# Optimization experiments

Measured on AMD Instinct MI355X. Metric: run time of the kernel, lower is better.

The kernel has to match this reference:

```python
import jax, jax.numpy as jnp
import numpy as np

# Fixed-step Dormand-Prince RK45 (dopri5) over t in [0, 1].
# torchdiffeq's dopri5 is adaptive; an adaptive while-loop is not
# reverse-differentiable in JAX, so we use the same dopri5 tableau with a
# fixed step count, which reproduces the per-step math exactly.
N_STEPS = 64

# dopri5 Butcher tableau (a-matrix rows; b = 5th-order weights = row a7)
A21 = 1/5
A31, A32 = 3/40, 9/40
A41, A42, A43 = 44/45, -56/15, 32/9
A51, A52, A53, A54 = 19372/6561, -25360/2187, 64448/6561, -212/729
A61, A62, A63, A64, A65 = 9017/3168, -355/33, 46732/5247, 49/176, -5103/18656
B1, B3, B4, B5, B6 = 35/384, 500/1113, 125/192, -2187/6784, 11/84


def setup_inputs() -> dict:
    key = jax.random.key(0)
    ks = jax.random.split(key, 7)
    data_dim, hidden_dim, batch = 512, 1024, 4096
    s1 = 1.0 / np.sqrt(data_dim)
    s2 = 1.0 / np.sqrt(hidden_dim)
    return {
        "x":  jax.random.normal(ks[0], (batch, data_dim), jnp.float32),
        "W1": jax.random.normal(ks[1], (hidden_dim, data_dim), jnp.float32) * s1,
        "b1": jax.random.normal(ks[2], (hidden_dim,), jnp.float32) * s1,
        "W2": jax.random.normal(ks[3], (hidden_dim, hidden_dim), jnp.float32) * s2,
        "b2": jax.random.normal(ks[4], (hidden_dim,), jnp.float32) * s2,
        "W3": jax.random.normal(ks[5], (data_dim, hidden_dim), jnp.float32) * s2,
        "b3": jax.random.normal(ks[6], (data_dim,), jnp.float32) * s2,
    }


def reference(x, W1, b1, W2, b2, W3, b3):
    def f(y):  # ODEFunc MLP: fc1 -> relu -> fc2 -> relu -> fc3 (autonomous)
        h = jax.nn.relu(y @ W1.T + b1)
        h = jax.nn.relu(h @ W2.T + b2)
        return h @ W3.T + b3

    h = jnp.float32(1.0 / N_STEPS)

    def step(y, _):
        k1 = f(y)
        k2 = f(y + h * (A21 * k1))
        k3 = f(y + h * (A31 * k1 + A32 * k2))
        k4 = f(y + h * (A41 * k1 + A42 * k2 + A43 * k3))
        k5 = f(y + h * (A51 * k1 + A52 * k2 + A53 * k3 + A54 * k4))
        k6 = f(y + h * (A61 * k1 + A62 * k2 + A63 * k3 + A64 * k4 + A65 * k5))
        y_next = y + h * (B1 * k1 + B3 * k3 + B4 * k4 + B5 * k5 + B6 * k6)
        return y_next, None

    y_final, _ = jax.lax.scan(step, x, None, length=N_STEPS)
    return y_final
```

## Files before the change

kernel.cpp:

```cpp
#include <hip/hip_runtime.h>
#include <hip/hip_bf16.h>
#include <stdint.h>
#include <stddef.h>

using bf16_t = __hip_bfloat16;
typedef __attribute__((ext_vector_type(8))) short short8;
typedef __attribute__((ext_vector_type(4))) float f32x4;

__device__ __forceinline__ void gload_lds16(void* lds, const void* g) {
  __builtin_amdgcn_global_load_lds(
      (const __attribute__((address_space(1))) unsigned int*)g,
      (__attribute__((address_space(3))) unsigned int*)lds,
      16, 0, 0);
}

template<int MODE>
__device__ __forceinline__ void gemm_core(
    const bf16_t* __restrict__ A, const bf16_t* __restrict__ B,
    const float* __restrict__ bias,
    bf16_t* __restrict__ obf,
    bf16_t* __restrict__ aux,
    bf16_t* __restrict__ vout,
    float* __restrict__ wacc,
    float* __restrict__ yf_out,
    const float* __restrict__ y_in,
    const bf16_t* __restrict__ p0, const bf16_t* __restrict__ p1,
    const bf16_t* __restrict__ p2, const bf16_t* __restrict__ p3,
    float c0, float c1, float c2, float c3, float ccur, int hinit,
    int M, int N, int K, int lgx)
{
  __shared__ __align__(16) bf16_t As[2][64 * 64];
  __shared__ __align__(16) bf16_t Bs[2][64 * 64];

  const int t    = threadIdx.x;
  const int lane = t & 63;
  const int wid  = t >> 6;
  const int wm   = wid >> 1;
  const int wn   = wid & 1;

  const int nwg = gridDim.x, bid = blockIdx.x;
  const int swz = (bid & 7) * (nwg >> 3) + (bid >> 3);
  const int gxm = (1 << lgx) - 1;
  const int bx  = swz & gxm;
  const int by  = swz >> lgx;
  const int bn0 = bx * 64, bm0 = by * 64;

  const bf16_t* Ag = A + (size_t)bm0 * K;
  const bf16_t* Bg = B + (size_t)bn0 * K;

  f32x4 acc[2][2] = {};

  auto stage = [&](int b, int kt) {
    const int k0 = kt * 64;
#pragma unroll
    for (int r = 0; r < 2; ++r) {
      int ch  = t + r * 256;
      int row = ch >> 3, s = ch & 7;
      int sl  = s ^ (row & 7);
      gload_lds16(&As[b][ch * 8], Ag + (size_t)row * K + k0 + sl * 8);
    }
#pragma unroll
    for (int r = 0; r < 2; ++r) {
      int ch  = t + r * 256;
      int row = ch >> 3, s = ch & 7;
      int sl  = s ^ (row & 7);
      gload_lds16(&Bs[b][ch * 8], Bg + (size_t)row * K + k0 + sl * 8);
    }
  };

  const int nt = K >> 6;
  stage(0, 0);

  const int ro = lane & 15;
  const int ks = lane >> 4;

  for (int tt = 0; tt < nt; ++tt) {
    const int c = tt & 1;
    asm volatile("s_waitcnt vmcnt(0)" ::: "memory");
    __builtin_amdgcn_s_barrier();
    asm volatile("" ::: "memory");
    if (tt + 1 < nt) stage(c ^ 1, tt + 1);

#pragma unroll
    for (int kk = 0; kk < 2; ++kk) {
      short8 af[2], bfr[2];
      const int slot = kk * 4 + ks;
#pragma unroll
      for (int mi = 0; mi < 2; ++mi) {
        int row = wm * 32 + mi * 16 + ro;
        int ch  = row * 8 + (slot ^ (row & 7));
        af[mi]  = *(const short8*)&As[c][ch * 8];
      }
#pragma unroll
      for (int ni = 0; ni < 2; ++ni) {
        int row = wn * 32 + ni * 16 + ro;
        int ch  = row * 8 + (slot ^ (row & 7));
        bfr[ni] = *(const short8*)&Bs[c][ch * 8];
      }
      __builtin_amdgcn_s_setprio(1);
#pragma unroll
      for (int mi = 0; mi < 2; ++mi)
#pragma unroll
        for (int ni = 0; ni < 2; ++ni)
          acc[mi][ni] = __builtin_amdgcn_mfma_f32_16x16x32_bf16(
              af[mi], bfr[ni], acc[mi][ni], 0, 0, 0);
      __builtin_amdgcn_s_setprio(0);
    }
  }

  const int rb = bm0 + wm * 32;
  const int cb = bn0 + wn * 32;
#pragma unroll
  for (int mi = 0; mi < 2; ++mi) {
#pragma unroll
    for (int ni = 0; ni < 2; ++ni) {
      const int col = cb + ni * 16 + ro;
      const float bv = bias ? bias[col] : 0.f;
#pragma unroll
      for (int r = 0; r < 4; ++r) {
        const int row = rb + mi * 16 + (lane >> 4) * 4 + r;
        const size_t idx = (size_t)row * N + col;
        const float a = acc[mi][ni][r];
        if (MODE == 0) {
          float v = fmaxf(a + bv, 0.f);
          obf[idx] = __float2bfloat16(v);
          if (aux) {
            float hs = ccur * v + (hinit ? 0.f : __bfloat162float(aux[idx]));
            aux[idx] = __float2bfloat16(hs);
          }
        } else if (MODE == 1) {
          vout[idx] = __float2bfloat16(a);
          float u = wacc[idx] + ccur * a + bv;
          if (p0) u += c0 * __bfloat162float(p0[idx]);
          if (p1) u += c1 * __bfloat162float(p1[idx]);
          if (p2) u += c2 * __bfloat162float(p2[idx]);
          if (p3) u += c3 * __bfloat162float(p3[idx]);
          obf[idx] = __float2bfloat16(fmaxf(u, 0.f));
        } else if (MODE == 2) {
          wacc[idx]   = a;
          yf_out[idx] = 0.f;
          obf[idx]    = __float2bfloat16(fmaxf(a + bv, 0.f));
        } else if (MODE == 3) {
          obf[idx] = __float2bfloat16(a);
        } else if (MODE == 4) {
          yf_out[idx] = y_in[idx] + a + ccur * bv;
        } else {
          float u = wacc[idx] + a + ccur * bv;
          wacc[idx] = u;
          yf_out[idx] += __bfloat162float(p0[idx]);
          obf[idx] = __float2bfloat16(fmaxf(u + y_in[col], 0.f));
        }
      }
    }
  }
}

#define GARGS                                                               \
    const bf16_t* A, const bf16_t* B, const float* bias, bf16_t* obf,       \
    bf16_t* aux, bf16_t* vout, float* wacc, float* yf_out,                  \
    const float* y_in,                                                      \
    const bf16_t* p0, const bf16_t* p1, const bf16_t* p2, const bf16_t* p3, \
    float c0, float c1, float c2, float c3, float ccur, int hinit,          \
    int M, int N, int K, int lgx
#define GPASS A,B,bias,obf,aux,vout,wacc,yf_out,y_in,p0,p1,p2,p3,c0,c1,c2,c3,ccur,hinit,M,N,K,lgx

extern "C" __global__ void __launch_bounds__(256, 4) gmid(GARGS) { gemm_core<0>(GPASS); }
extern "C" __global__ void __launch_bounds__(256, 4) gvst(GARGS) { gemm_core<1>(GPASS); }
extern "C" __global__ void __launch_bounds__(256, 4) gyw1(GARGS) { gemm_core<2>(GPASS); }
extern "C" __global__ void __launch_bounds__(256, 4) gw13(GARGS) { gemm_core<3>(GPASS); }
extern "C" __global__ void __launch_bounds__(256, 4) gfin(GARGS) { gemm_core<4>(GPASS); }
extern "C" __global__ void __launch_bounds__(256, 4) gs1v(GARGS) { gemm_core<5>(GPASS); }

extern "C" __global__ void init_all(
    const float* __restrict__ x,
    const float* __restrict__ W1, const float* __restrict__ W2,
    const float* __restrict__ W3,
    const float* __restrict__ b1, const float* __restrict__ b3,
    bf16_t* __restrict__ W1b, bf16_t* __restrict__ W2b,
    bf16_t* __restrict__ W3b, bf16_t* __restrict__ W3Tb,
    bf16_t* __restrict__ yb,
    float* __restrict__ c13f,
    float* __restrict__ bS2, float* __restrict__ bS3, float* __restrict__ bS4,
    float* __restrict__ bS5, float* __restrict__ bS6,
    float s2, float s3, float s4, float s5, float s6)
{
  const int gt = blockIdx.x * blockDim.x + threadIdx.x;
  const int gs = gridDim.x * blockDim.x;
  auto cvt4 = [&](const float* in, bf16_t* outp, int n) {
    for (int i = gt * 4; i < n; i += gs * 4) {
      float4 v = *(const float4*)(in + i);
      bf16_t o[4] = {__float2bfloat16(v.x), __float2bfloat16(v.y),
                     __float2bfloat16(v.z), __float2bfloat16(v.w)};
      *(uint64_t*)(outp + i) = *(uint64_t*)o;
    }
  };
  cvt4(W1, W1b, 1024 * 512);
  cvt4(W2, W2b, 1024 * 1024);
  cvt4(W3, W3b, 512 * 1024);
  cvt4(x, (bf16_t*)yb, 4096 * 512);
  for (int i = gt; i < 512 * 1024; i += gs) {
    int d = i >> 10, j = i & 1023;
    W3Tb[(size_t)j * 512 + d] = __float2bfloat16(W3[i]);
  }
  if (gt < 1024) {
    float c13 = 0.f;
    const float* wr = W1 + (size_t)gt * 512;
    for (int d = 0; d < 512; ++d) c13 += b3[d] * wr[d];
    const float bb = b1[gt];
    c13f[gt] = c13;
    bS2[gt] = bb + s2 * c13;
    bS3[gt] = bb + s3 * c13;
    bS4[gt] = bb + s4 * c13;
    bS5[gt] = bb + s5 * c13;
    bS6[gt] = bb + s6 * c13;
  }
}

extern "C" __global__ void ewfin(const float* __restrict__ Stot,
                                 const bf16_t* __restrict__ hsum,
                                 bf16_t* __restrict__ Stotb, int n)
{
  const int gt = blockIdx.x * blockDim.x + threadIdx.x;
  const int gs = gridDim.x * blockDim.x;
  for (int i = gt * 4; i < n; i += gs * 4) {
    float4 s = *(const float4*)(Stot + i);
    uint64_t hv = *(const uint64_t*)(hsum + i);
    const bf16_t* hp = (const bf16_t*)&hv;
    bf16_t o[4];
    o[0] = __float2bfloat16(s.x + __bfloat162float(hp[0]));
    o[1] = __float2bfloat16(s.y + __bfloat162float(hp[1]));
    o[2] = __float2bfloat16(s.z + __bfloat162float(hp[2]));
    o[3] = __float2bfloat16(s.w + __bfloat162float(hp[3]));
    *(uint64_t*)(Stotb + i) = *(uint64_t*)o;
  }
}

extern "C" void kernel_launch(void* const* d_in, const int* in_sizes, int n_in,
                              void* d_out, int out_size, void* d_ws, size_t ws_size,
                              hipStream_t stream)
{
  const float* x  = (const float*)d_in[0];
  const float* W1 = (const float*)d_in[1];
  const float* b1 = (const float*)d_in[2];
  const float* W2 = (const float*)d_in[3];
  const float* b2 = (const float*)d_in[4];
  const float* W3 = (const float*)d_in[5];
  const float* b3 = (const float*)d_in[6];

  constexpr int BATCH = 4096, DATA = 512, HID = 1024;

  char* ws = (char*)d_ws;
  size_t off = 0;
  auto alloc = [&](size_t bytes) -> void* {
    off = (off + 255) & ~(size_t)255;
    void* p = ws + off;
    off += bytes;
    return p;
  };
  const size_t nyd = (size_t)BATCH * DATA;
  const size_t nh  = (size_t)BATCH * HID;

  bf16_t* yb   = (bf16_t*)alloc(nyd * 2);
  bf16_t* h1b  = (bf16_t*)alloc(nh * 2);
  bf16_t* h2b  = (bf16_t*)alloc(nh * 2);
  float*  yw1f = (float*)alloc(nh * 4);
  float*  Stot = (float*)alloc(nh * 4);
  bf16_t* Stotb= (bf16_t*)alloc(nh * 2);
  bf16_t* hsumb= (bf16_t*)alloc(nh * 2);
  bf16_t* v1   = (bf16_t*)alloc(nh * 2);
  bf16_t* v2   = (bf16_t*)alloc(nh * 2);
  bf16_t* v3   = (bf16_t*)alloc(nh * 2);
  bf16_t* v4   = (bf16_t*)alloc(nh * 2);
  bf16_t* v5   = (bf16_t*)alloc(nh * 2);
  bf16_t* W1b  = (bf16_t*)alloc((size_t)HID * DATA * 2);
  bf16_t* W2b  = (bf16_t*)alloc((size_t)HID * HID * 2);
  bf16_t* W3b  = (bf16_t*)alloc((size_t)DATA * HID * 2);
  bf16_t* W3Tb = (bf16_t*)alloc((size_t)HID * DATA * 2);
  bf16_t* W13b = (bf16_t*)alloc((size_t)HID * HID * 2);
  float*  c13f = (float*)alloc(HID * 4);
  float*  bS2  = (float*)alloc(HID * 4);
  float*  bS3  = (float*)alloc(HID * 4);
  float*  bS4  = (float*)alloc(HID * 4);
  float*  bS5  = (float*)alloc(HID * 4);
  float*  bS6  = (float*)alloc(HID * 4);

  const double hh = 1.0 / 64.0;
  const float hA21 = (float)(hh * (1.0/5.0));
  const float hA31 = (float)(hh * (3.0/40.0)),    hA32 = (float)(hh * (9.0/40.0));
  const float hA41 = (float)(hh * (44.0/45.0)),   hA42 = (float)(hh * (-56.0/15.0)),
              hA43 = (float)(hh * (32.0/9.0));
  const float hA51 = (float)(hh * (19372.0/6561.0)),  hA52 = (float)(hh * (-25360.0/2187.0)),
              hA53 = (float)(hh * (64448.0/6561.0)),  hA54 = (float)(hh * (-212.0/729.0));
  const float hA61 = (float)(hh * (9017.0/3168.0)),   hA62 = (float)(hh * (-355.0/33.0)),
              hA63 = (float)(hh * (46732.0/5247.0)),  hA64 = (float)(hh * (49.0/176.0)),
              hA65 = (float)(hh * (-5103.0/18656.0));
  const float hB1 = (float)(hh * (35.0/384.0)),   hB3 = (float)(hh * (500.0/1113.0)),
              hB4 = (float)(hh * (125.0/192.0)),  hB5 = (float)(hh * (-2187.0/6784.0)),
              hB6 = (float)(hh * (11.0/84.0));
  const float s2 = hA21, s3 = hA31 + hA32, s4 = hA41 + hA42 + hA43,
              s5 = hA51 + hA52 + hA53 + hA54,
              s6 = hA61 + hA62 + hA63 + hA64 + hA65;

  init_all<<<2048, 256, 0, stream>>>(x, W1, W2, W3, b1, b3,
                                     W1b, W2b, W3b, W3Tb, yb,
                                     c13f, bS2, bS3, bS4, bS5, bS6,
                                     s2, s3, s4, s5, s6);

  const dim3 blk(256);
  const int gridN = (HID / 64) * (BATCH / 64);
  const int gridY = (DATA / 64) * (BATCH / 64);
  const int gridW = (HID / 64) * (HID / 64);

  gw13<<<gridW, blk, 0, stream>>>(
      W1b, W3Tb, nullptr, W13b, nullptr, nullptr, nullptr, nullptr, nullptr,
      nullptr, nullptr, nullptr, nullptr, 0.f, 0.f, 0.f, 0.f, 0.f, 0,
      HID, HID, DATA, 4);

  auto G2 = [&](bf16_t* hs, float coef, int hinit) {
    gmid<<<gridN, blk, 0, stream>>>(
        h1b, W2b, b2, h2b, hs, nullptr, nullptr, nullptr, nullptr,
        nullptr, nullptr, nullptr, nullptr,
        0.f, 0.f, 0.f, 0.f, coef, hinit, BATCH, HID, HID, 4);
  };
  auto V = [&](bf16_t* vo, const float* bS, float ccur,
               const bf16_t* q0, float cc0, const bf16_t* q1, float cc1,
               const bf16_t* q2, float cc2, const bf16_t* q3, float cc3) {
    gvst<<<gridN, blk, 0, stream>>>(
        h2b, W13b, bS, h1b, nullptr, vo, yw1f, nullptr, nullptr,
        q0, q1, q2, q3, cc0, cc1, cc2, cc3, ccur, 0, BATCH, HID, HID, 4);
  };

  for (int step = 0; step < 64; ++step) {
    if (step == 0) {
      gyw1<<<gridN, blk, 0, stream>>>(
          yb, W1b, b1, h1b, nullptr, nullptr, yw1f, Stot, nullptr,
          nullptr, nullptr, nullptr, nullptr,
          0.f, 0.f, 0.f, 0.f, 0.f, 0, BATCH, HID, DATA, 4);
    } else {
      gs1v<<<gridN, blk, 0, stream>>>(
          hsumb, W13b, c13f, h1b, nullptr, nullptr, yw1f, Stot, b1,
          hsumb, nullptr, nullptr, nullptr,
          0.f, 0.f, 0.f, 0.f, (float)hh, 0, BATCH, HID, HID, 4);
    }
    G2(hsumb, hB1, 1);
    V(v1, bS2, hA21, nullptr,0,nullptr,0,nullptr,0,nullptr,0);
    G2(nullptr, 0.f, 0);
    V(v2, bS3, hA32, v1,hA31, nullptr,0,nullptr,0,nullptr,0);
    G2(hsumb, hB3, 0);
    V(v3, bS4, hA43, v1,hA41, v2,hA42, nullptr,0,nullptr,0);
    G2(hsumb, hB4, 0);
    V(v4, bS5, hA54, v1,hA51, v2,hA52, v3,hA53, nullptr,0);
    G2(hsumb, hB5, 0);
    V(v5, bS6, hA65, v1,hA61, v2,hA62, v3,hA63, v4,hA64);
    G2(hsumb, hB6, 0);
  }

  ewfin<<<1024, 256, 0, stream>>>(Stot, hsumb, Stotb, (int)nh);
  gfin<<<gridY, blk, 0, stream>>>(
      Stotb, W3b, b3, nullptr, nullptr, nullptr, nullptr, (float*)d_out, x,
      nullptr, nullptr, nullptr, nullptr,
      0.f, 0.f, 0.f, 0.f, 1.0f, 0, BATCH, DATA, HID, 3);
}
```

Before: 17.68 ms.

## Pre-pack weights into MFMA fragment layout, load B directly to registers, 128-row tiles

Weights are repacked once into a per-lane MFMA fragment layout so each wave loads its B operands straight from global memory into registers, which removes the B shared-memory staging. The M tile doubles to 128 rows with a 4x2 accumulator per wave, and the K loop is unrolled by two with double-buffered register B fragments. Launch bounds drop to 2 blocks per CU. The aim is to cut LDS traffic and barrier cost per MFMA; the trade-off is higher register pressure, fewer blocks in the grid, and an extra packing pass for W13.

```diff
diff --git a/kernel.cpp b/kernel.cpp
--- a/kernel.cpp
+++ b/kernel.cpp
@@ -16,7 +16,7 @@
 
 template<int MODE>
 __device__ __forceinline__ void gemm_core(
-    const bf16_t* __restrict__ A, const bf16_t* __restrict__ B,
+    const bf16_t* __restrict__ A, const bf16_t* __restrict__ Bp,
     const float* __restrict__ bias,
     bf16_t* __restrict__ obf,
     bf16_t* __restrict__ aux,
@@ -29,8 +29,7 @@
     float c0, float c1, float c2, float c3, float ccur, int hinit,
     int M, int N, int K, int lgx)
 {
-  __shared__ __align__(16) bf16_t As[2][64 * 64];
-  __shared__ __align__(16) bf16_t Bs[2][64 * 64];
+  __shared__ __align__(16) bf16_t As[2][128 * 64];
 
   const int t    = threadIdx.x;
   const int lane = t & 63;
@@ -43,75 +42,84 @@
   const int gxm = (1 << lgx) - 1;
   const int bx  = swz & gxm;
   const int by  = swz >> lgx;
-  const int bn0 = bx * 64, bm0 = by * 64;
+  const int bn0 = bx * 64, bm0 = by * 128;
 
   const bf16_t* Ag = A + (size_t)bm0 * K;
-  const bf16_t* Bg = B + (size_t)bn0 * K;
-
-  f32x4 acc[2][2] = {};
-
-  auto stage = [&](int b, int kt) {
+  const int ntk = K >> 6;
+  const bf16_t* Bw = Bp + ((size_t)(bx * 4 + wn * 2) * ntk * 2) * 512
+                        + (size_t)lane * 8;
+
+  auto stageA = [&](int b, int kt) {
     const int k0 = kt * 64;
 #pragma unroll
-    for (int r = 0; r < 2; ++r) {
+    for (int r = 0; r < 4; ++r) {
       int ch  = t + r * 256;
       int row = ch >> 3, s = ch & 7;
       int sl  = s ^ (row & 7);
       gload_lds16(&As[b][ch * 8], Ag + (size_t)row * K + k0 + sl * 8);
     }
-#pragma unroll
-    for (int r = 0; r < 2; ++r) {
-      int ch  = t + r * 256;
-      int row = ch >> 3, s = ch & 7;
-      int sl  = s ^ (row & 7);
-      gload_lds16(&Bs[b][ch * 8], Bg + (size_t)row * K + k0 + sl * 8);
-    }
-  };
-
-  const int nt = K >> 6;
-  stage(0, 0);
-
+  };
+  auto loadB = [&](short8* dst, int kt) {
+#pragma unroll
+    for (int ni = 0; ni < 2; ++ni)
+#pragma unroll
+      for (int kk = 0; kk < 2; ++kk)
+        dst[ni * 2 + kk] = *(const short8*)
+            (Bw + ((size_t)ni * ntk * 2 + kt * 2 + kk) * 512);
+  };
+
+  f32x4 acc[4][2] = {};
   const int ro = lane & 15;
   const int ks = lane >> 4;
 
-  for (int tt = 0; tt < nt; ++tt) {
-    const int c = tt & 1;
-    asm volatile("s_waitcnt vmcnt(0)" ::: "memory");
+  auto compute = [&](const bf16_t* lds, const short8* bfr) {
+#pragma unroll
+    for (int kk = 0; kk < 2; ++kk) {
+      short8 af[4];
+      const int slot = kk * 4 + ks;
+#pragma unroll
+      for (int mi = 0; mi < 4; ++mi) {
+        int row = wm * 64 + mi * 16 + ro;
+        int ch  = row * 8 + (slot ^ (row & 7));
+        af[mi]  = *(const short8*)&lds[ch * 8];
+      }
+      __builtin_amdgcn_s_setprio(1);
+#pragma unroll
+      for (int mi = 0; mi < 4; ++mi)
+#pragma unroll
+        for (int ni = 0; ni < 2; ++ni)
+          acc[mi][ni] = __builtin_amdgcn_mfma_f32_16x16x32_bf16(
+              af[mi], bfr[ni * 2 + kk], acc[mi][ni], 0, 0, 0);
+      __builtin_amdgcn_s_setprio(0);
+    }
+  };
+
+  short8 b0[4], b1[4];
+  stageA(0, 0);
+  loadB(b0, 0);
+
+  for (int tt = 0; tt < ntk; tt += 2) {
+    asm volatile("s_waitcnt vmcnt(4)" ::: "memory");
     __builtin_amdgcn_s_barrier();
     asm volatile("" ::: "memory");
-    if (tt + 1 < nt) stage(c ^ 1, tt + 1);
-
-#pragma unroll
-    for (int kk = 0; kk < 2; ++kk) {
-      short8 af[2], bfr[2];
-      const int slot = kk * 4 + ks;
-#pragma unroll
-      for (int mi = 0; mi < 2; ++mi) {
-        int row = wm * 32 + mi * 16 + ro;
-        int ch  = row * 8 + (slot ^ (row & 7));
-        af[mi]  = *(const short8*)&As[c][ch * 8];
-      }
-#pragma unroll
-      for (int ni = 0; ni < 2; ++ni) {
-        int row = wn * 32 + ni * 16 + ro;
-        int ch  = row * 8 + (slot ^ (row & 7));
-        bfr[ni] = *(const short8*)&Bs[c][ch * 8];
-      }
-      __builtin_amdgcn_s_setprio(1);
-#pragma unroll
-      for (int mi = 0; mi < 2; ++mi)
-#pragma unroll
-        for (int ni = 0; ni < 2; ++ni)
-          acc[mi][ni] = __builtin_amdgcn_mfma_f32_16x16x32_bf16(
-              af[mi], bfr[ni], acc[mi][ni], 0, 0, 0);
-      __builtin_amdgcn_s_setprio(0);
-    }
-  }
-
-  const int rb = bm0 + wm * 32;
+    stageA(1, tt + 1);
+    loadB(b1, tt + 1);
+    compute(As[0], b0);
+
+    asm volatile("s_waitcnt vmcnt(4)" ::: "memory");
+    __builtin_amdgcn_s_barrier();
+    asm volatile("" ::: "memory");
+    if (tt + 2 < ntk) {
+      stageA(0, tt + 2);
+      loadB(b0, tt + 2);
+    }
+    compute(As[1], b1);
+  }
+
+  const int rb = bm0 + wm * 64;
   const int cb = bn0 + wn * 32;
 #pragma unroll
-  for (int mi = 0; mi < 2; ++mi) {
+  for (int mi = 0; mi < 4; ++mi) {
 #pragma unroll
     for (int ni = 0; ni < 2; ++ni) {
       const int col = cb + ni * 16 + ro;
@@ -164,21 +172,58 @@
     int M, int N, int K, int lgx
 #define GPASS A,B,bias,obf,aux,vout,wacc,yf_out,y_in,p0,p1,p2,p3,c0,c1,c2,c3,ccur,hinit,M,N,K,lgx
 
-extern "C" __global__ void __launch_bounds__(256, 4) gmid(GARGS) { gemm_core<0>(GPASS); }
-extern "C" __global__ void __launch_bounds__(256, 4) gvst(GARGS) { gemm_core<1>(GPASS); }
-extern "C" __global__ void __launch_bounds__(256, 4) gyw1(GARGS) { gemm_core<2>(GPASS); }
-extern "C" __global__ void __launch_bounds__(256, 4) gw13(GARGS) { gemm_core<3>(GPASS); }
-extern "C" __global__ void __launch_bounds__(256, 4) gfin(GARGS) { gemm_core<4>(GPASS); }
-extern "C" __global__ void __launch_bounds__(256, 4) gs1v(GARGS) { gemm_core<5>(GPASS); }
+extern "C" __global__ void __launch_bounds__(256, 2) gmid(GARGS) { gemm_core<0>(GPASS); }
+extern "C" __global__ void __launch_bounds__(256, 2) gvst(GARGS) { gemm_core<1>(GPASS); }
+extern "C" __global__ void __launch_bounds__(256, 2) gyw1(GARGS) { gemm_core<2>(GPASS); }
+extern "C" __global__ void __launch_bounds__(256, 2) gw13(GARGS) { gemm_core<3>(GPASS); }
+extern "C" __global__ void __launch_bounds__(256, 2) gfin(GARGS) { gemm_core<4>(GPASS); }
+extern "C" __global__ void __launch_bounds__(256, 2) gs1v(GARGS) { gemm_core<5>(GPASS); }
+
+__device__ __forceinline__ void pack_w(const float* __restrict__ W,
+                                       bf16_t* __restrict__ Wp,
+                                       int N, int K, int gt, int gs)
+{
+  const int nchunk = (N * K) / 8;
+  const int ktn = K >> 6;
+  for (int c = gt; c < nchunk; c += gs) {
+    int lane = c & 63, kk = (c >> 6) & 1, kt = (c >> 7) % ktn;
+    int ntile = c / (ktn * 128);
+    const float* src = W + (size_t)(ntile * 16 + (lane & 15)) * K
+                         + kt * 64 + kk * 32 + (lane >> 4) * 8;
+    bf16_t o[8];
+#pragma unroll
+    for (int j = 0; j < 8; ++j) o[j] = __float2bfloat16(src[j]);
+    *(short8*)(Wp + (size_t)c * 8) = *(short8*)o;
+  }
+}
+
+__device__ __forceinline__ void pack_wT(const float* __restrict__ W3,
+                                        bf16_t* __restrict__ Wp,
+                                        int gt, int gs)
+{
+  const int nchunk = (1024 * 512) / 8;
+  const int ktn = 8;
+  for (int c = gt; c < nchunk; c += gs) {
+    int lane = c & 63, kk = (c >> 6) & 1, kt = (c >> 7) % ktn;
+    int ntile = c / (ktn * 128);
+    int jrow = ntile * 16 + (lane & 15);
+    int dcol = kt * 64 + kk * 32 + (lane >> 4) * 8;
+    bf16_t o[8];
+#pragma unroll
+    for (int j = 0; j < 8; ++j)
+      o[j] = __float2bfloat16(W3[(size_t)(dcol + j) * 1024 + jrow]);
+    *(short8*)(Wp + (size_t)c * 8) = *(short8*)o;
+  }
+}
 
 extern "C" __global__ void init_all(
     const float* __restrict__ x,
     const float* __restrict__ W1, const float* __restrict__ W2,
     const float* __restrict__ W3,
     const float* __restrict__ b1, const float* __restrict__ b3,
-    bf16_t* __restrict__ W1b, bf16_t* __restrict__ W2b,
-    bf16_t* __restrict__ W3b, bf16_t* __restrict__ W3Tb,
-    bf16_t* __restrict__ yb,
+    bf16_t* __restrict__ W1b,  bf16_t* __restrict__ W1p,
+    bf16_t* __restrict__ W2p,  bf16_t* __restrict__ W3p,
+    bf16_t* __restrict__ W3Tp, bf16_t* __restrict__ yb,
     float* __restrict__ c13f,
     float* __restrict__ bS2, float* __restrict__ bS3, float* __restrict__ bS4,
     float* __restrict__ bS5, float* __restrict__ bS6,
@@ -195,13 +240,11 @@
     }
   };
   cvt4(W1, W1b, 1024 * 512);
-  cvt4(W2, W2b, 1024 * 1024);
-  cvt4(W3, W3b, 512 * 1024);
-  cvt4(x, (bf16_t*)yb, 4096 * 512);
-  for (int i = gt; i < 512 * 1024; i += gs) {
-    int d = i >> 10, j = i & 1023;
-    W3Tb[(size_t)j * 512 + d] = __float2bfloat16(W3[i]);
-  }
+  cvt4(x, yb, 4096 * 512);
+  pack_w(W1, W1p, 1024, 512, gt, gs);
+  pack_w(W2, W2p, 1024, 1024, gt, gs);
+  pack_w(W3, W3p, 512, 1024, gt, gs);
+  pack_wT(W3, W3Tp, gt, gs);
   if (gt < 1024) {
     float c13 = 0.f;
     const float* wr = W1 + (size_t)gt * 512;
@@ -213,6 +256,22 @@
     bS4[gt] = bb + s4 * c13;
     bS5[gt] = bb + s5 * c13;
     bS6[gt] = bb + s6 * c13;
+  }
+}
+
+extern "C" __global__ void packw13(const bf16_t* __restrict__ W,
+                                   bf16_t* __restrict__ Wp)
+{
+  const int gt = blockIdx.x * blockDim.x + threadIdx.x;
+  const int gs = gridDim.x * blockDim.x;
+  const int ktn = 16;
+  const int nchunk = (1024 * 1024) / 8;
+  for (int c = gt; c < nchunk; c += gs) {
+    int lane = c & 63, kk = (c >> 6) & 1, kt = (c >> 7) % ktn;
+    int ntile = c / (ktn * 128);
+    const bf16_t* src = W + (size_t)(ntile * 16 + (lane & 15)) * 1024
+                          + kt * 64 + kk * 32 + (lane >> 4) * 8;
+    *(short8*)(Wp + (size_t)c * 8) = *(const short8*)src;
   }
 }
 
@@ -273,10 +332,12 @@
   bf16_t* v4   = (bf16_t*)alloc(nh * 2);
   bf16_t* v5   = (bf16_t*)alloc(nh * 2);
   bf16_t* W1b  = (bf16_t*)alloc((size_t)HID * DATA * 2);
-  bf16_t* W2b  = (bf16_t*)alloc((size_t)HID * HID * 2);
-  bf16_t* W3b  = (bf16_t*)alloc((size_t)DATA * HID * 2);
-  bf16_t* W3Tb = (bf16_t*)alloc((size_t)HID * DATA * 2);
+  bf16_t* W1p  = (bf16_t*)alloc((size_t)HID * DATA * 2);
+  bf16_t* W2p  = (bf16_t*)alloc((size_t)HID * HID * 2);
+  bf16_t* W3p  = (bf16_t*)alloc((size_t)DATA * HID * 2);
+  bf16_t* W3Tp = (bf16_t*)alloc((size_t)HID * DATA * 2);
   bf16_t* W13b = (bf16_t*)alloc((size_t)HID * HID * 2);
+  bf16_t* W13p = (bf16_t*)alloc((size_t)HID * HID * 2);
   float*  c13f = (float*)alloc(HID * 4);
   float*  bS2  = (float*)alloc(HID * 4);
   float*  bS3  = (float*)alloc(HID * 4);
@@ -302,23 +363,24 @@
               s6 = hA61 + hA62 + hA63 + hA64 + hA65;
 
   init_all<<<2048, 256, 0, stream>>>(x, W1, W2, W3, b1, b3,
-                                     W1b, W2b, W3b, W3Tb, yb,
+                                     W1b, W1p, W2p, W3p, W3Tp, yb,
                                      c13f, bS2, bS3, bS4, bS5, bS6,
                                      s2, s3, s4, s5, s6);
 
   const dim3 blk(256);
-  const int gridN = (HID / 64) * (BATCH / 64);
-  const int gridY = (DATA / 64) * (BATCH / 64);
-  const int gridW = (HID / 64) * (HID / 64);
+  const int gridN = (HID / 64) * (BATCH / 128);
+  const int gridY = (DATA / 64) * (BATCH / 128);
+  const int gridW = (HID / 64) * (HID / 128);
 
   gw13<<<gridW, blk, 0, stream>>>(
-      W1b, W3Tb, nullptr, W13b, nullptr, nullptr, nullptr, nullptr, nullptr,
+      W1b, W3Tp, nullptr, W13b, nullptr, nullptr, nullptr, nullptr, nullptr,
       nullptr, nullptr, nullptr, nullptr, 0.f, 0.f, 0.f, 0.f, 0.f, 0,
       HID, HID, DATA, 4);
+  packw13<<<2048, 256, 0, stream>>>(W13b, W13p);
 
   auto G2 = [&](bf16_t* hs, float coef, int hinit) {
     gmid<<<gridN, blk, 0, stream>>>(
-        h1b, W2b, b2, h2b, hs, nullptr, nullptr, nullptr, nullptr,
+        h1b, W2p, b2, h2b, hs, nullptr, nullptr, nullptr, nullptr,
         nullptr, nullptr, nullptr, nullptr,
         0.f, 0.f, 0.f, 0.f, coef, hinit, BATCH, HID, HID, 4);
   };
@@ -326,19 +388,19 @@
                const bf16_t* q0, float cc0, const bf16_t* q1, float cc1,
                const bf16_t* q2, float cc2, const bf16_t* q3, float cc3) {
     gvst<<<gridN, blk, 0, stream>>>(
-        h2b, W13b, bS, h1b, nullptr, vo, yw1f, nullptr, nullptr,
+        h2b, W13p, bS, h1b, nullptr, vo, yw1f, nullptr, nullptr,
         q0, q1, q2, q3, cc0, cc1, cc2, cc3, ccur, 0, BATCH, HID, HID, 4);
   };
 
   for (int step = 0; step < 64; ++step) {
     if (step == 0) {
       gyw1<<<gridN, blk, 0, stream>>>(
-          yb, W1b, b1, h1b, nullptr, nullptr, yw1f, Stot, nullptr,
+          yb, W1p, b1, h1b, nullptr, nullptr, yw1f, Stot, nullptr,
           nullptr, nullptr, nullptr, nullptr,
           0.f, 0.f, 0.f, 0.f, 0.f, 0, BATCH, HID, DATA, 4);
     } else {
       gs1v<<<gridN, blk, 0, stream>>>(
-          hsumb, W13b, c13f, h1b, nullptr, nullptr, yw1f, Stot, b1,
+          hsumb, W13p, c13f, h1b, nullptr, nullptr, yw1f, Stot, b1,
           hsumb, nullptr, nullptr, nullptr,
           0.f, 0.f, 0.f, 0.f, (float)hh, 0, BATCH, HID, HID, 4);
     }
@@ -357,7 +419,7 @@
 
   ewfin<<<1024, 256, 0, stream>>>(Stot, hsumb, Stotb, (int)nh);
   gfin<<<gridY, blk, 0, stream>>>(
-      Stotb, W3b, b3, nullptr, nullptr, nullptr, nullptr, (float*)d_out, x,
+      Stotb, W3p, b3, nullptr, nullptr, nullptr, nullptr, (float*)d_out, x,
       nullptr, nullptr, nullptr, nullptr,
       0.f, 0.f, 0.f, 0.f, 1.0f, 0, BATCH, DATA, HID, 3);
 }
```

After: 21.93 ms. 1.24x slower.
